# Kernel tuning notes

Measured on AMD Instinct MI355X. Metric: run time of the kernel, lower is better.

The kernel has to match this reference:

```python
import jax, jax.numpy as jnp
import numpy as np

B, N, D = 8, 2048, 512   # batch, ctx_size, input_size
P, H = 16, 32            # num_pers, hidden_size


def setup_inputs() -> dict:
    key = jax.random.key(0)
    k1, k2 = jax.random.split(key)
    context = jax.random.normal(k1, (B, N, D), dtype=jnp.float32)
    # stacked weights of the 16 bias-free nn.Linear(input_size, hidden_size) layers
    # xavier-uniform-style scale: sqrt(6/(fan_in+fan_out))
    limit = np.sqrt(6.0 / (D + H)).astype(np.float32)
    W = jax.random.uniform(k2, (P, H, D), dtype=jnp.float32, minval=-limit, maxval=limit)
    ctx_mask = jnp.ones((B, N), dtype=jnp.int32)
    return {"context": context, "W": W, "ctx_mask": ctx_mask}


def reference(context, W, ctx_mask):
    # per-persona projection + relu: [P, B, N, H]
    fc = jax.nn.relu(jnp.einsum('bnd,phd->pbnh', context, W))
    # sum over personas of fc @ fc^T, then average: [B, N, N]
    att = jnp.einsum('pbnh,pbmh->bnm', fc, fc) / P
    # NOTE: original uses F.softmax(attention, dim=1) -> softmax over rows (axis=1)
    att = jax.nn.softmax(att, axis=1)
    # masked_fill with markoff_value=0 on masked columns then masked rows
    m = ctx_mask.astype(att.dtype)          # [B, N]
    att = att * m[:, None, :] * m[:, :, None]
    return att
```

## Files before the change

kernel.cpp:

```cpp
#include <hip/hip_runtime.h>

#define Bc 8
#define Nc 2048
#define Dc 512
#define PH 512
#define NN 4194304
#define NT 136

#define BM 128
#define BN 128
#define BK 32

typedef __attribute__((ext_vector_type(8))) short bf16x8;
typedef __attribute__((ext_vector_type(4))) float f32x4;

static __device__ __forceinline__ unsigned short f2b(float x) {
    union { float f; unsigned u; } v; v.f = x;
    unsigned r = v.u + 0x7fffu + ((v.u >> 16) & 1u);
    return (unsigned short)(r >> 16);
}

static __device__ __forceinline__ float b2f(unsigned short x) {
    return __builtin_bit_cast(float, (unsigned)x << 16);
}

static __device__ __forceinline__ unsigned pk2(float lo, float hi) {
    unsigned r;
    asm("v_cvt_pk_bf16_f32 %0, %1, %2" : "=v"(r) : "v"(lo), "v"(hi));
    return r;
}

static __device__ __forceinline__ void load16_lds(const unsigned short* g, unsigned short* l) {
    __builtin_amdgcn_global_load_lds(
        (const __attribute__((address_space(1))) void*)g,
        (__attribute__((address_space(3))) void*)l,
        16, 0, 0);
}

__global__ __launch_bounds__(256) void gemm1_fused(
    const float* __restrict__ ctx, const float* __restrict__ W,
    unsigned short* __restrict__ F) {
    __shared__ unsigned short As[BM * BK];
    __shared__ unsigned short Bs[BN * BK];
    const int tid = threadIdx.x;
    const int lane = tid & 63;
    const int wave = tid >> 6;
    const int wm = wave >> 1, wn = wave & 1;
    const int bid = blockIdx.x;
    const int row0 = ((bid & 7) + ((bid >> 5) << 3)) * BM;
    const int col0 = ((bid >> 3) & 3) * BN;

    f32x4 acc[4][4] = {};

    for (int k0 = 0; k0 < Dc; k0 += BK) {
        int4 aw[2], bw[2];
#pragma unroll
        for (int j = 0; j < 2; ++j) {
            int e = j * 256 + tid;
            int rr = e >> 2, cc = e & 3;
            const float4* ga = (const float4*)&ctx[(size_t)(row0 + rr) * Dc + k0 + cc * 8];
            const float4* gb = (const float4*)&W[(size_t)(col0 + rr) * Dc + k0 + cc * 8];
            float4 a0 = ga[0], a1 = ga[1];
            float4 b0 = gb[0], b1 = gb[1];
            aw[j].x = pk2(a0.x, a0.y); aw[j].y = pk2(a0.z, a0.w);
            aw[j].z = pk2(a1.x, a1.y); aw[j].w = pk2(a1.z, a1.w);
            bw[j].x = pk2(b0.x, b0.y); bw[j].y = pk2(b0.z, b0.w);
            bw[j].z = pk2(b1.x, b1.y); bw[j].w = pk2(b1.z, b1.w);
        }
#pragma unroll
        for (int j = 0; j < 2; ++j) {
            int e = j * 256 + tid;
            *(int4*)&As[e * 8] = aw[j];
            *(int4*)&Bs[e * 8] = bw[j];
        }
        __syncthreads();

        bf16x8 af[4], bfr[4];
#pragma unroll
        for (int i = 0; i < 4; ++i) {
            af[i]  = *(const bf16x8*)&As[(wm * 64 + i * 16 + (lane & 15)) * BK + (lane >> 4) * 8];
            bfr[i] = *(const bf16x8*)&Bs[(wn * 64 + i * 16 + (lane & 15)) * BK + (lane >> 4) * 8];
        }
#pragma unroll
        for (int mi = 0; mi < 4; ++mi)
#pragma unroll
            for (int ni = 0; ni < 4; ++ni)
                acc[mi][ni] = __builtin_amdgcn_mfma_f32_16x16x32_bf16(af[mi], bfr[ni], acc[mi][ni], 0, 0, 0);
        __syncthreads();
    }

#pragma unroll
    for (int mi = 0; mi < 4; ++mi) {
#pragma unroll
        for (int ni = 0; ni < 4; ++ni) {
            int col  = col0 + wn * 64 + ni * 16 + (lane & 15);
            int rowb = row0 + wm * 64 + mi * 16 + ((lane >> 4) << 2);
#pragma unroll
            for (int r = 0; r < 4; ++r) {
                float v = fmaxf(acc[mi][ni][r], 0.0f);
                F[(size_t)(rowb + r) * PH + col] = f2b(v);
            }
        }
    }
}

__global__ __launch_bounds__(256) void gemm2_store(
    const unsigned short* __restrict__ F, float* __restrict__ rsum,
    unsigned short* __restrict__ Ework) {
    __shared__ unsigned short As[BM * BK];
    __shared__ unsigned short Bs[BN * BK];
    const int tid = threadIdx.x;
    const int lane = tid & 63;
    const int wave = tid >> 6;
    const int wm = wave >> 1, wn = wave & 1;
    const int l15 = lane & 15, q = lane >> 4;
    const int b = blockIdx.x & 7;
    const int idx = blockIdx.x >> 3;

    int j = 0;
    while (((j + 1) * (j + 2) / 2) <= idx) ++j;
    int i = idx - j * (j + 1) / 2;
    const int row0 = i * BM;
    const int col0 = j * BN;
    const bool offd = (i != j);
    const unsigned short* Fb = F + (size_t)b * Nc * PH;

    f32x4 acc[4][4] = {};

    for (int k0 = 0; k0 < PH; k0 += BK) {
#pragma unroll
        for (int jj = 0; jj < 2; ++jj) {
            int e = jj * 256 + tid;
            int rr = e >> 2, cc = e & 3;
            load16_lds(&Fb[(size_t)(row0 + rr) * PH + k0 + cc * 8], &As[e * 8]);
            if (offd)
                load16_lds(&Fb[(size_t)(col0 + rr) * PH + k0 + cc * 8], &Bs[e * 8]);
        }
        __syncthreads();

        bf16x8 af[4], bfr[4];
#pragma unroll
        for (int qq = 0; qq < 4; ++qq)
            af[qq] = *(const bf16x8*)&As[(wm * 64 + qq * 16 + l15) * BK + q * 8];
        if (offd) {
#pragma unroll
            for (int qq = 0; qq < 4; ++qq)
                bfr[qq] = *(const bf16x8*)&Bs[(wn * 64 + qq * 16 + l15) * BK + q * 8];
        } else {
#pragma unroll
            for (int qq = 0; qq < 4; ++qq)
                bfr[qq] = *(const bf16x8*)&As[(wn * 64 + qq * 16 + l15) * BK + q * 8];
        }
#pragma unroll
        for (int mi = 0; mi < 4; ++mi)
#pragma unroll
            for (int ni = 0; ni < 4; ++ni)
                acc[mi][ni] = __builtin_amdgcn_mfma_f32_16x16x32_bf16(af[mi], bfr[ni], acc[mi][ni], 0, 0, 0);
        __syncthreads();
    }

    unsigned short* Et = Ework + (size_t)(b * NT + idx) * 16384;

    float csum[4] = {0.f, 0.f, 0.f, 0.f};
    float rsm[4][4];
#pragma unroll
    for (int mi = 0; mi < 4; ++mi)
#pragma unroll
        for (int r = 0; r < 4; ++r) rsm[mi][r] = 0.f;

#pragma unroll
    for (int mi = 0; mi < 4; ++mi) {
#pragma unroll
        for (int ni = 0; ni < 4; ++ni) {
#pragma unroll
            for (int r = 0; r < 4; ++r) {
                float e = __expf(acc[mi][ni][r] * 0.0625f - 32.0f);
                Et[(wm * 64 + mi * 16 + (q << 2) + r) * 128 + wn * 64 + ni * 16 + l15] = f2b(e);
                csum[ni] += e;
                rsm[mi][r] += e;
            }
        }
    }
#pragma unroll
    for (int ni = 0; ni < 4; ++ni) {
        float s = csum[ni];
        s += __shfl_xor(s, 16);
        s += __shfl_xor(s, 32);
        if ((lane >> 4) == 0)
            atomicAdd(&rsum[b * Nc + col0 + wn * 64 + ni * 16 + lane], s);
    }
    if (offd) {
#pragma unroll
        for (int mi = 0; mi < 4; ++mi) {
#pragma unroll
            for (int r = 0; r < 4; ++r) {
                float s = rsm[mi][r];
                s += __shfl_xor(s, 1);
                s += __shfl_xor(s, 2);
                s += __shfl_xor(s, 4);
                s += __shfl_xor(s, 8);
                if ((lane & 15) == 0)
                    atomicAdd(&rsum[b * Nc + row0 + wm * 64 + mi * 16 + ((lane >> 4) << 2) + r], s);
            }
        }
    }
}

__global__ __launch_bounds__(256) void scatter_out(
    const unsigned short* __restrict__ Ework, const float* __restrict__ rsum,
    const int* __restrict__ mask, float* __restrict__ out) {
    __shared__ float Ts[32 * 132];
    __shared__ float invA[128];
    __shared__ float invB[128];
    const int tid = threadIdx.x;
    const int b = blockIdx.x & 7;
    const int idx = blockIdx.x >> 3;

    int j = 0;
    while (((j + 1) * (j + 2) / 2) <= idx) ++j;
    int i = idx - j * (j + 1) / 2;
    const int row0 = i * BM;
    const int col0 = j * BN;

    const unsigned short* Et = Ework + (size_t)(b * NT + idx) * 16384;
    const float* rsb  = rsum + b * Nc;
    const int*   mb   = mask + b * Nc;
    float* outb = out + (size_t)b * NN;

    if (tid < 128)       invA[tid]       = (float)mb[col0 + tid]       / rsb[col0 + tid];
    else                 invB[tid - 128] = (float)mb[row0 + tid - 128] / rsb[row0 + tid - 128];
    __syncthreads();

    const int cl = tid >> 3, f0 = tid & 7;
    const int mc = tid >> 1, h  = tid & 1;

    for (int ci = 0; ci < 4; ++ci) {
        if (ci) __syncthreads();
        const int r = ci * 32 + cl;
        const int n = row0 + r;
        const float mrow = (float)mb[n];
#pragma unroll
        for (int g = 0; g < 2; ++g) {
            const int c0 = 64 * g + 8 * f0;
            union { int4 iv; unsigned short hv[8]; } u;
            u.iv = *(const int4*)&Et[r * 128 + c0];
            float ev[8];
#pragma unroll
            for (int k = 0; k < 8; ++k) ev[k] = b2f(u.hv[k]);
            *(float4*)&Ts[cl * 132 + c0]     = *(float4*)&ev[0];
            *(float4*)&Ts[cl * 132 + c0 + 4] = *(float4*)&ev[4];
            float4 iv0 = *(const float4*)&invA[c0];
            float4 iv1 = *(const float4*)&invA[c0 + 4];
            float4 o0, o1;
            o0.x = ev[0] * iv0.x * mrow;
            o0.y = ev[1] * iv0.y * mrow;
            o0.z = ev[2] * iv0.z * mrow;
            o0.w = ev[3] * iv0.w * mrow;
            o1.x = ev[4] * iv1.x * mrow;
            o1.y = ev[5] * iv1.y * mrow;
            o1.z = ev[6] * iv1.z * mrow;
            o1.w = ev[7] * iv1.w * mrow;
            *(float4*)&outb[(size_t)n * Nc + col0 + c0]     = o0;
            *(float4*)&outb[(size_t)n * Nc + col0 + c0 + 4] = o1;
        }
        if (i == j) continue;
        __syncthreads();
        const int a = col0 + mc;
        const float mcol = (float)mb[a];
        const int lb0 = ci * 32 + 16 * h;
        const int nb0 = row0 + lb0;
#pragma unroll
        for (int u = 0; u < 4; ++u) {
            float4 iv = *(const float4*)&invB[lb0 + 4 * u];
            float4 o;
            o.x = Ts[(16 * h + 4 * u + 0) * 132 + mc] * iv.x * mcol;
            o.y = Ts[(16 * h + 4 * u + 1) * 132 + mc] * iv.y * mcol;
            o.z = Ts[(16 * h + 4 * u + 2) * 132 + mc] * iv.z * mcol;
            o.w = Ts[(16 * h + 4 * u + 3) * 132 + mc] * iv.w * mcol;
            *(float4*)&outb[(size_t)a * Nc + nb0 + 4 * u] = o;
        }
    }
}

__global__ __launch_bounds__(256) void prep_kernel(
    const float* __restrict__ ctx, const float* __restrict__ W,
    unsigned short* __restrict__ Xb, unsigned short* __restrict__ Wb,
    float* __restrict__ rsum) {
    int t = blockIdx.x * 256 + threadIdx.x;
    if (t < 2097152) {
        float4 v = ((const float4*)ctx)[t];
        ushort4 o;
        o.x = f2b(v.x); o.y = f2b(v.y); o.z = f2b(v.z); o.w = f2b(v.w);
        ((ushort4*)Xb)[t] = o;
    }
    if (t < 65536) {
        float4 v = ((const float4*)W)[t];
        ushort4 o;
        o.x = f2b(v.x); o.y = f2b(v.y); o.z = f2b(v.z); o.w = f2b(v.w);
        ((ushort4*)Wb)[t] = o;
    }
    if (t < 4096) {
        float4 z; z.x = 0.f; z.y = 0.f; z.z = 0.f; z.w = 0.f;
        ((float4*)rsum)[t] = z;
    }
}

__global__ __launch_bounds__(256) void invr_kernel(
    const float* __restrict__ rsum, const int* __restrict__ mask,
    float* __restrict__ invr) {
    int t = blockIdx.x * 256 + threadIdx.x;
    if (t < Bc * Nc) invr[t] = (float)mask[t] / rsum[t];
}

__global__ __launch_bounds__(256) void gemm1_relu_fb(
    const unsigned short* __restrict__ Xb, const unsigned short* __restrict__ Wb,
    unsigned short* __restrict__ F) {
    __shared__ unsigned short As[BM * BK];
    __shared__ unsigned short Bs[BN * BK];
    const int tid = threadIdx.x;
    const int lane = tid & 63;
    const int wave = tid >> 6;
    const int wm = wave >> 1, wn = wave & 1;
    const int row0 = blockIdx.y * BM;
    const int col0 = blockIdx.x * BN;

    f32x4 acc[4][4] = {};

    for (int k0 = 0; k0 < Dc; k0 += BK) {
#pragma unroll
        for (int j = 0; j < 2; ++j) {
            int e = j * 256 + tid;
            int rr = e >> 2, cc = e & 3;
            load16_lds(&Xb[(size_t)(row0 + rr) * Dc + k0 + cc * 8], &As[e * 8]);
            load16_lds(&Wb[(size_t)(col0 + rr) * Dc + k0 + cc * 8], &Bs[e * 8]);
        }
        __syncthreads();

        bf16x8 af[4], bfr[4];
#pragma unroll
        for (int i = 0; i < 4; ++i) {
            af[i]  = *(const bf16x8*)&As[(wm * 64 + i * 16 + (lane & 15)) * BK + (lane >> 4) * 8];
            bfr[i] = *(const bf16x8*)&Bs[(wn * 64 + i * 16 + (lane & 15)) * BK + (lane >> 4) * 8];
        }
#pragma unroll
        for (int mi = 0; mi < 4; ++mi)
#pragma unroll
            for (int ni = 0; ni < 4; ++ni)
                acc[mi][ni] = __builtin_amdgcn_mfma_f32_16x16x32_bf16(af[mi], bfr[ni], acc[mi][ni], 0, 0, 0);
        __syncthreads();
    }

#pragma unroll
    for (int mi = 0; mi < 4; ++mi) {
#pragma unroll
        for (int ni = 0; ni < 4; ++ni) {
            int col  = col0 + wn * 64 + ni * 16 + (lane & 15);
            int rowb = row0 + wm * 64 + mi * 16 + ((lane >> 4) << 2);
#pragma unroll
            for (int r = 0; r < 4; ++r) {
                float v = fmaxf(acc[mi][ni][r], 0.0f);
                F[(size_t)(rowb + r) * PH + col] = f2b(v);
            }
        }
    }
}

__global__ __launch_bounds__(256) void gemm2_rsum(
    const unsigned short* __restrict__ F, float* __restrict__ rsum) {
    __shared__ unsigned short As[BM * BK];
    __shared__ unsigned short Bs[BN * BK];
    const int tid = threadIdx.x;
    const int lane = tid & 63;
    const int wave = tid >> 6;
    const int wm = wave >> 1, wn = wave & 1;
    const int b = blockIdx.y;

    int idx = blockIdx.x;
    int j = 0;
    while (((j + 1) * (j + 2) / 2) <= idx) ++j;
    int i = idx - j * (j + 1) / 2;
    const int row0 = i * BM;
    const int col0 = j * BN;
    const unsigned short* Fb = F + (size_t)b * Nc * PH;

    f32x4 acc[4][4] = {};

    for (int k0 = 0; k0 < PH; k0 += BK) {
#pragma unroll
        for (int jj = 0; jj < 2; ++jj) {
            int e = jj * 256 + tid;
            int rr = e >> 2, cc = e & 3;
            load16_lds(&Fb[(size_t)(row0 + rr) * PH + k0 + cc * 8], &As[e * 8]);
            load16_lds(&Fb[(size_t)(col0 + rr) * PH + k0 + cc * 8], &Bs[e * 8]);
        }
        __syncthreads();

        bf16x8 af[4], bfr[4];
#pragma unroll
        for (int q = 0; q < 4; ++q) {
            af[q]  = *(const bf16x8*)&As[(wm * 64 + q * 16 + (lane & 15)) * BK + (lane >> 4) * 8];
            bfr[q] = *(const bf16x8*)&Bs[(wn * 64 + q * 16 + (lane & 15)) * BK + (lane >> 4) * 8];
        }
#pragma unroll
        for (int mi = 0; mi < 4; ++mi)
#pragma unroll
            for (int ni = 0; ni < 4; ++ni)
                acc[mi][ni] = __builtin_amdgcn_mfma_f32_16x16x32_bf16(af[mi], bfr[ni], acc[mi][ni], 0, 0, 0);
        __syncthreads();
    }

    float csum[4] = {0.f, 0.f, 0.f, 0.f};
    float rsm[4][4];
#pragma unroll
    for (int mi = 0; mi < 4; ++mi)
#pragma unroll
        for (int r = 0; r < 4; ++r) rsm[mi][r] = 0.f;

#pragma unroll
    for (int mi = 0; mi < 4; ++mi) {
#pragma unroll
        for (int ni = 0; ni < 4; ++ni) {
#pragma unroll
            for (int r = 0; r < 4; ++r) {
                float e = __expf(acc[mi][ni][r] * 0.0625f - 32.0f);
                csum[ni] += e;
                rsm[mi][r] += e;
            }
        }
    }
#pragma unroll
    for (int ni = 0; ni < 4; ++ni) {
        float s = csum[ni];
        s += __shfl_xor(s, 16);
        s += __shfl_xor(s, 32);
        if ((lane >> 4) == 0)
            atomicAdd(&rsum[b * Nc + col0 + wn * 64 + ni * 16 + lane], s);
    }
    if (i != j) {
#pragma unroll
        for (int mi = 0; mi < 4; ++mi) {
#pragma unroll
            for (int r = 0; r < 4; ++r) {
                float s = rsm[mi][r];
                s += __shfl_xor(s, 1);
                s += __shfl_xor(s, 2);
                s += __shfl_xor(s, 4);
                s += __shfl_xor(s, 8);
                if ((lane & 15) == 0)
                    atomicAdd(&rsum[b * Nc + row0 + wm * 64 + mi * 16 + ((lane >> 4) << 2) + r], s);
            }
        }
    }
}

__global__ __launch_bounds__(256) void gemm2_write_sym(
    const unsigned short* __restrict__ F, const float* __restrict__ invr,
    const int* __restrict__ mask, float* __restrict__ out) {
    __shared__ unsigned short As[BM * BK];
    __shared__ unsigned short Bs[BN * BK];
    __shared__ float Ts[32 * 132];
    const int tid = threadIdx.x;
    const int lane = tid & 63;
    const int wave = tid >> 6;
    const int wm = wave >> 1, wn = wave & 1;
    const int l15 = lane & 15, q = lane >> 4;
    const int b = blockIdx.y;

    int idx = blockIdx.x;
    int j = 0;
    while (((j + 1) * (j + 2) / 2) <= idx) ++j;
    int i = idx - j * (j + 1) / 2;
    const int row0 = i * BM;
    const int col0 = j * BN;
    const unsigned short* Fb = F + (size_t)b * Nc * PH;

    f32x4 acc[4][4] = {};

    for (int k0 = 0; k0 < PH; k0 += BK) {
#pragma unroll
        for (int jj = 0; jj < 2; ++jj) {
            int e = jj * 256 + tid;
            int rr = e >> 2, cc = e & 3;
            load16_lds(&Fb[(size_t)(row0 + rr) * PH + k0 + cc * 8], &As[e * 8]);
            load16_lds(&Fb[(size_t)(col0 + rr) * PH + k0 + cc * 8], &Bs[e * 8]);
        }
        __syncthreads();

        bf16x8 af[4], bfr[4];
#pragma unroll
        for (int qq = 0; qq < 4; ++qq) {
            af[qq]  = *(const bf16x8*)&As[(wm * 64 + qq * 16 + l15) * BK + q * 8];
            bfr[qq] = *(const bf16x8*)&Bs[(wn * 64 + qq * 16 + l15) * BK + q * 8];
        }
#pragma unroll
        for (int mi = 0; mi < 4; ++mi)
#pragma unroll
            for (int ni = 0; ni < 4; ++ni)
                acc[mi][ni] = __builtin_amdgcn_mfma_f32_16x16x32_bf16(af[mi], bfr[ni], acc[mi][ni], 0, 0, 0);
        __syncthreads();
    }

#pragma unroll
    for (int mi = 0; mi < 4; ++mi)
#pragma unroll
        for (int ni = 0; ni < 4; ++ni)
#pragma unroll
            for (int r = 0; r < 4; ++r)
                acc[mi][ni][r] = __expf(acc[mi][ni][r] * 0.0625f - 32.0f);

    float* outb = out + (size_t)b * NN;

    float iv[4];
#pragma unroll
    for (int ni = 0; ni < 4; ++ni)
        iv[ni] = invr[b * Nc + col0 + wn * 64 + ni * 16 + l15];
#pragma unroll
    for (int mi = 0; mi < 4; ++mi) {
        int rowb = row0 + wm * 64 + mi * 16 + (q << 2);
        const int4 mr4 = *(const int4*)&mask[b * Nc + rowb];
        float mr[4] = {(float)mr4.x, (float)mr4.y, (float)mr4.z, (float)mr4.w};
#pragma unroll
        for (int ni = 0; ni < 4; ++ni) {
            int col = col0 + wn * 64 + ni * 16 + l15;
#pragma unroll
            for (int r = 0; r < 4; ++r)
                outb[(size_t)(rowb + r) * Nc + col] = acc[mi][ni][r] * iv[ni] * mr[r];
        }
    }

    if (i != j) {
#pragma unroll
        for (int ci = 0; ci < 4; ++ci) {
            __syncthreads();
            if (wn == (ci >> 1)) {
#pragma unroll
                for (int ni2 = 0; ni2 < 2; ++ni2) {
                    int ni = (ci & 1) * 2 + ni2;
#pragma unroll
                    for (int mi = 0; mi < 4; ++mi) {
                        *(float4*)&Ts[(ni2 * 16 + l15) * 132 + wm * 64 + mi * 16 + (q << 2)] =
                            *(float4*)&acc[mi][ni];
                    }
                }
            }
            __syncthreads();
            int cl = tid >> 3;
            int f0 = tid & 7;
            int nn = col0 + ci * 32 + cl;
            float mrow = (float)mask[b * Nc + nn];
            float* orow = &outb[(size_t)nn * Nc + row0];
#pragma unroll
            for (int g = 0; g < 4; ++g) {
                int f = f0 + g * 8;
                float4 ev  = *(float4*)&Ts[cl * 132 + 4 * f];
                float4 iv4 = *(const float4*)&invr[b * Nc + row0 + 4 * f];
                float4 o;
                o.x = ev.x * iv4.x * mrow;
                o.y = ev.y * iv4.y * mrow;
                o.z = ev.z * iv4.z * mrow;
                o.w = ev.w * iv4.w * mrow;
                *(float4*)&orow[4 * f] = o;
            }
        }
    }
}

extern "C" void kernel_launch(void* const* d_in, const int* in_sizes, int n_in,
                              void* d_out, int out_size, void* d_ws, size_t ws_size,
                              hipStream_t stream) {
    const float* ctx  = (const float*)d_in[0];
    const float* W    = (const float*)d_in[1];
    const int*   mask = (const int*)d_in[2];
    float* out = (float*)d_out;

    char* ws = (char*)d_ws;

    const size_t NEED = 52494336;

    if (ws_size >= NEED) {
        unsigned short* Ework = (unsigned short*)ws;
        unsigned short* F     = (unsigned short*)(ws + 35651584);
        float*          rsum  = (float*)(ws + 52428800);

        hipMemsetAsync(rsum, 0, Bc * Nc * sizeof(float), stream);
        gemm1_fused<<<512, 256, 0, stream>>>(ctx, W, F);
        gemm2_store<<<1088, 256, 0, stream>>>(F, rsum, Ework);
        scatter_out<<<1088, 256, 0, stream>>>(Ework, rsum, mask, out);
    } else {
        unsigned short* Xb = (unsigned short*)ws;
        unsigned short* Wb = (unsigned short*)(ws + 16777216);
        unsigned short* F  = (unsigned short*)(ws + 16777216 + 524288);
        float* rsum        = (float*)(ws + 16777216 + 524288 + 16777216);
        float* invr        = (float*)(ws + 16777216 + 524288 + 16777216 + 65536);

        prep_kernel<<<8192, 256, 0, stream>>>(ctx, W, Xb, Wb, rsum);
        gemm1_relu_fb<<<dim3(4, 128), 256, 0, stream>>>(Xb, Wb, F);
        gemm2_rsum<<<dim3(136, 8), 256, 0, stream>>>(F, rsum);
        invr_kernel<<<64, 256, 0, stream>>>(rsum, mask, invr);
        gemm2_write_sym<<<dim3(136, 8), 256, 0, stream>>>(F, invr, mask, out);
    }
}
```

Measured before the change: 230.4 us.

## Fuse gram GEMM, softmax sums and output scatter into one cooperative persistent kernel

Replaces the separate gemm2_store and scatter_out launches with one cooperative persistent kernel. Blocks grab symmetric tiles through atomic counters, compute the exp and column/row sums, and stash earlier tiles as bf16 while keeping the last tile in registers. After a grid-wide sync they write the normalized output and its mirrored transpose. The aim is to avoid writing and re-reading the full bf16 intermediate for the register-resident tile and to save a launch, at the cost of grid sync overhead, a capped occupancy of 4 blocks per SM, and a fallback path if the cooperative launch fails.

```diff
diff --git a/kernel.cpp b/kernel.cpp
--- a/kernel.cpp
+++ b/kernel.cpp
@@ -1,4 +1,7 @@
 #include <hip/hip_runtime.h>
+#include <hip/hip_cooperative_groups.h>
+
+namespace cg = cooperative_groups;
 
 #define Bc 8
 #define Nc 2048
@@ -99,6 +102,272 @@
             for (int r = 0; r < 4; ++r) {
                 float v = fmaxf(acc[mi][ni][r], 0.0f);
                 F[(size_t)(rowb + r) * PH + col] = f2b(v);
+            }
+        }
+    }
+}
+
+__global__ __launch_bounds__(256, 4) void gemm2_fused(
+    const unsigned short* __restrict__ F, float* __restrict__ rsum,
+    unsigned int* __restrict__ ctrs, unsigned short* __restrict__ Estash,
+    const int* __restrict__ mask, float* __restrict__ out) {
+    __shared__ __align__(16) char smem[17920];
+    __shared__ int tshare, sshare;
+    unsigned short* As = (unsigned short*)smem;
+    unsigned short* Bs = (unsigned short*)(smem + 8192);
+    float* Ts   = (float*)smem;
+    float* invA = (float*)(smem + 16896);
+    float* invB = (float*)(smem + 17408);
+
+    const int tid = threadIdx.x;
+    const int lane = tid & 63;
+    const int wave = tid >> 6;
+    const int wm = wave >> 1, wn = wave & 1;
+    const int l15 = lane & 15, q = lane >> 4;
+    const int pref = blockIdx.x & 7;
+
+    f32x4 acc[4][4];
+    int ownT[4], ownS[4];
+    int nT = 0;
+
+    for (int iter = 0; iter < 4; ++iter) {
+        int tb = -1, ti = 0;
+#pragma unroll 1
+        for (int d = 0; d < 8; ++d) {
+            const int bb = (pref + d) & 7;
+            __syncthreads();
+            if (tid == 0) tshare = (int)atomicAdd(&ctrs[bb], 1u);
+            __syncthreads();
+            const int v = tshare;
+            if (v < NT) { tb = bb; ti = v; break; }
+        }
+        if (tb < 0) break;
+
+        if (nT > 0) {
+            if (tid == 0) sshare = (int)atomicAdd(&ctrs[8], 1u);
+            __syncthreads();
+            const int slot = sshare;
+            ownS[nT - 1] = slot;
+            unsigned short* Et = Estash + (size_t)slot * 16384;
+#pragma unroll
+            for (int mi = 0; mi < 4; ++mi)
+#pragma unroll
+                for (int ni = 0; ni < 4; ++ni)
+#pragma unroll
+                    for (int r = 0; r < 4; ++r)
+                        Et[(wm * 64 + mi * 16 + (q << 2) + r) * 128 + wn * 64 + ni * 16 + l15] =
+                            f2b(acc[mi][ni][r]);
+        }
+
+        int j = 0;
+        while (((j + 1) * (j + 2) / 2) <= ti) ++j;
+        const int i = ti - j * (j + 1) / 2;
+        const int row0 = i * BM, col0 = j * BN;
+        const bool offd = (i != j);
+        const unsigned short* Fb = F + (size_t)tb * Nc * PH;
+
+#pragma unroll
+        for (int mi = 0; mi < 4; ++mi)
+#pragma unroll
+            for (int ni = 0; ni < 4; ++ni) {
+                f32x4 z = {0.f, 0.f, 0.f, 0.f};
+                acc[mi][ni] = z;
+            }
+
+        for (int k0 = 0; k0 < PH; k0 += BK) {
+#pragma unroll
+            for (int jj = 0; jj < 2; ++jj) {
+                int e = jj * 256 + tid;
+                int rr = e >> 2, cc = e & 3;
+                load16_lds(&Fb[(size_t)(row0 + rr) * PH + k0 + cc * 8], &As[e * 8]);
+                if (offd)
+                    load16_lds(&Fb[(size_t)(col0 + rr) * PH + k0 + cc * 8], &Bs[e * 8]);
+            }
+            __syncthreads();
+
+            bf16x8 af[4], bfr[4];
+#pragma unroll
+            for (int qq = 0; qq < 4; ++qq)
+                af[qq] = *(const bf16x8*)&As[(wm * 64 + qq * 16 + l15) * BK + q * 8];
+            if (offd) {
+#pragma unroll
+                for (int qq = 0; qq < 4; ++qq)
+                    bfr[qq] = *(const bf16x8*)&Bs[(wn * 64 + qq * 16 + l15) * BK + q * 8];
+            } else {
+#pragma unroll
+                for (int qq = 0; qq < 4; ++qq)
+                    bfr[qq] = *(const bf16x8*)&As[(wn * 64 + qq * 16 + l15) * BK + q * 8];
+            }
+#pragma unroll
+            for (int mi = 0; mi < 4; ++mi)
+#pragma unroll
+                for (int ni = 0; ni < 4; ++ni)
+                    acc[mi][ni] = __builtin_amdgcn_mfma_f32_16x16x32_bf16(af[mi], bfr[ni], acc[mi][ni], 0, 0, 0);
+            __syncthreads();
+        }
+
+        float csum[4] = {0.f, 0.f, 0.f, 0.f};
+        float rsm[4][4];
+#pragma unroll
+        for (int mi = 0; mi < 4; ++mi)
+#pragma unroll
+            for (int r = 0; r < 4; ++r) rsm[mi][r] = 0.f;
+
+#pragma unroll
+        for (int mi = 0; mi < 4; ++mi) {
+#pragma unroll
+            for (int ni = 0; ni < 4; ++ni) {
+#pragma unroll
+                for (int r = 0; r < 4; ++r) {
+                    float e = __expf(acc[mi][ni][r] * 0.0625f - 32.0f);
+                    acc[mi][ni][r] = e;
+                    csum[ni] += e;
+                    rsm[mi][r] += e;
+                }
+            }
+        }
+#pragma unroll
+        for (int ni = 0; ni < 4; ++ni) {
+            float s = csum[ni];
+            s += __shfl_xor(s, 16);
+            s += __shfl_xor(s, 32);
+            if ((lane >> 4) == 0)
+                atomicAdd(&rsum[tb * Nc + col0 + wn * 64 + ni * 16 + lane], s);
+        }
+        if (offd) {
+#pragma unroll
+            for (int mi = 0; mi < 4; ++mi) {
+#pragma unroll
+                for (int r = 0; r < 4; ++r) {
+                    float s = rsm[mi][r];
+                    s += __shfl_xor(s, 1);
+                    s += __shfl_xor(s, 2);
+                    s += __shfl_xor(s, 4);
+                    s += __shfl_xor(s, 8);
+                    if ((lane & 15) == 0)
+                        atomicAdd(&rsum[tb * Nc + row0 + wm * 64 + mi * 16 + ((lane >> 4) << 2) + r], s);
+                }
+            }
+        }
+        ownT[nT++] = (tb << 16) | ti;
+    }
+
+    cg::this_grid().sync();
+
+    const int cl = tid >> 3, f0 = tid & 7;
+    const int mc = tid >> 1, h  = tid & 1;
+
+    for (int s = 0; s < nT; ++s) {
+        const int tb = ownT[s] >> 16, ti = ownT[s] & 0xffff;
+        int j = 0;
+        while (((j + 1) * (j + 2) / 2) <= ti) ++j;
+        const int i = ti - j * (j + 1) / 2;
+        const int row0 = i * BM, col0 = j * BN;
+        const float* rsb = rsum + tb * Nc;
+        const int*   mb  = mask + tb * Nc;
+        float* outb = out + (size_t)tb * NN;
+
+        __syncthreads();
+        if (tid < 128) invA[tid]       = (float)mb[col0 + tid]       / rsb[col0 + tid];
+        else           invB[tid - 128] = (float)mb[row0 + tid - 128] / rsb[row0 + tid - 128];
+        __syncthreads();
+
+        if (s == nT - 1) {
+            float iv[4];
+#pragma unroll
+            for (int ni = 0; ni < 4; ++ni) iv[ni] = invA[wn * 64 + ni * 16 + l15];
+#pragma unroll
+            for (int mi = 0; mi < 4; ++mi) {
+                int rowb = row0 + wm * 64 + mi * 16 + (q << 2);
+                const int4 mr4 = *(const int4*)&mb[rowb];
+                float mr[4] = {(float)mr4.x, (float)mr4.y, (float)mr4.z, (float)mr4.w};
+#pragma unroll
+                for (int ni = 0; ni < 4; ++ni) {
+                    int col = col0 + wn * 64 + ni * 16 + l15;
+#pragma unroll
+                    for (int r = 0; r < 4; ++r)
+                        outb[(size_t)(rowb + r) * Nc + col] = acc[mi][ni][r] * iv[ni] * mr[r];
+                }
+            }
+            if (i != j) {
+#pragma unroll
+                for (int ci = 0; ci < 4; ++ci) {
+                    __syncthreads();
+                    if (wn == (ci >> 1)) {
+#pragma unroll
+                        for (int ni2 = 0; ni2 < 2; ++ni2) {
+                            int ni = (ci & 1) * 2 + ni2;
+#pragma unroll
+                            for (int mi = 0; mi < 4; ++mi)
+                                *(float4*)&Ts[(ni2 * 16 + l15) * 132 + wm * 64 + mi * 16 + (q << 2)] =
+                                    *(float4*)&acc[mi][ni];
+                        }
+                    }
+                    __syncthreads();
+                    int nn = col0 + ci * 32 + cl;
+                    float mrow = (float)mb[nn];
+                    float* orow = &outb[(size_t)nn * Nc + row0];
+#pragma unroll
+                    for (int g = 0; g < 4; ++g) {
+                        int f = f0 + g * 8;
+                        float4 ev  = *(float4*)&Ts[cl * 132 + 4 * f];
+                        float4 iv4 = *(const float4*)&invB[4 * f];
+                        float4 o;
+                        o.x = ev.x * iv4.x * mrow;
+                        o.y = ev.y * iv4.y * mrow;
+                        o.z = ev.z * iv4.z * mrow;
+                        o.w = ev.w * iv4.w * mrow;
+                        *(float4*)&orow[4 * f] = o;
+                    }
+                }
+            }
+        } else {
+            const unsigned short* Et = Estash + (size_t)ownS[s] * 16384;
+            for (int ci = 0; ci < 4; ++ci) {
+                if (ci) __syncthreads();
+                const int r = ci * 32 + cl;
+                const int n = row0 + r;
+                const float mrow = (float)mb[n];
+#pragma unroll
+                for (int g = 0; g < 2; ++g) {
+                    const int c0 = 64 * g + 8 * f0;
+                    union { int4 iv; unsigned short hv[8]; } u;
+                    u.iv = *(const int4*)&Et[r * 128 + c0];
+                    float ev[8];
+#pragma unroll
+                    for (int k = 0; k < 8; ++k) ev[k] = b2f(u.hv[k]);
+                    *(float4*)&Ts[cl * 132 + c0]     = *(float4*)&ev[0];
+                    *(float4*)&Ts[cl * 132 + c0 + 4] = *(float4*)&ev[4];
+                    float4 iv0 = *(const float4*)&invA[c0];
+                    float4 iv1 = *(const float4*)&invA[c0 + 4];
+                    float4 o0, o1;
+                    o0.x = ev[0] * iv0.x * mrow;
+                    o0.y = ev[1] * iv0.y * mrow;
+                    o0.z = ev[2] * iv0.z * mrow;
+                    o0.w = ev[3] * iv0.w * mrow;
+                    o1.x = ev[4] * iv1.x * mrow;
+                    o1.y = ev[5] * iv1.y * mrow;
+                    o1.z = ev[6] * iv1.z * mrow;
+                    o1.w = ev[7] * iv1.w * mrow;
+                    *(float4*)&outb[(size_t)n * Nc + col0 + c0]     = o0;
+                    *(float4*)&outb[(size_t)n * Nc + col0 + c0 + 4] = o1;
+                }
+                if (i == j) continue;
+                __syncthreads();
+                const int a = col0 + mc;
+                const float mcol = (float)mb[a];
+                const int lb0 = ci * 32 + 16 * h;
+                const int nb0 = row0 + lb0;
+#pragma unroll
+                for (int u2 = 0; u2 < 4; ++u2) {
+                    float4 iv = *(const float4*)&invB[lb0 + 4 * u2];
+                    float4 o;
+                    o.x = Ts[(16 * h + 4 * u2 + 0) * 132 + mc] * iv.x * mcol;
+                    o.y = Ts[(16 * h + 4 * u2 + 1) * 132 + mc] * iv.y * mcol;
+                    o.z = Ts[(16 * h + 4 * u2 + 2) * 132 + mc] * iv.z * mcol;
+                    o.w = Ts[(16 * h + 4 * u2 + 3) * 132 + mc] * iv.w * mcol;
+                    *(float4*)&outb[(size_t)a * Nc + nb0 + 4 * u2] = o;
+                }
             }
         }
     }
@@ -575,17 +844,27 @@
 
     char* ws = (char*)d_ws;
 
-    const size_t NEED = 52494336;
+    const size_t NEED = 52494400;
 
     if (ws_size >= NEED) {
-        unsigned short* Ework = (unsigned short*)ws;
-        unsigned short* F     = (unsigned short*)(ws + 35651584);
-        float*          rsum  = (float*)(ws + 52428800);
-
-        hipMemsetAsync(rsum, 0, Bc * Nc * sizeof(float), stream);
+        unsigned short* Estash = (unsigned short*)ws;
+        unsigned short* F      = (unsigned short*)(ws + 35651584);
+        float*          rsum   = (float*)(ws + 52428800);
+        unsigned int*   ctrs   = (unsigned int*)(ws + 52494336);
+
+        hipMemsetAsync(rsum, 0, 65536 + 64, stream);
         gemm1_fused<<<512, 256, 0, stream>>>(ctx, W, F);
-        gemm2_store<<<1088, 256, 0, stream>>>(F, rsum, Ework);
-        scatter_out<<<1088, 256, 0, stream>>>(Ework, rsum, mask, out);
+
+        void* kargs[] = {(void*)&F, (void*)&rsum, (void*)&ctrs,
+                         (void*)&Estash, (void*)&mask, (void*)&out};
+        hipError_t cerr = hipLaunchCooperativeKernel(
+            reinterpret_cast<const void*>(&gemm2_fused),
+            dim3(1024), dim3(256), kargs, 0, stream);
+        if (cerr != hipSuccess) {
+            (void)hipGetLastError();
+            gemm2_store<<<1088, 256, 0, stream>>>(F, rsum, Estash);
+            scatter_out<<<1088, 256, 0, stream>>>(Estash, rsum, mask, out);
+        }
     } else {
         unsigned short* Xb = (unsigned short*)ws;
         unsigned short* Wb = (unsigned short*)(ws + 16777216);
```

Measured after the change: 433.6 us. 88.2% more time.
